# Optimization experiments

Measured on AMD Instinct MI355X. Metric: run time of the kernel, lower is better.

## Reference

```python
import jax, jax.numpy as jnp
import numpy as np

B, S, H, A = 2, 1024, 512, 128


def setup_inputs() -> dict:
    key = jax.random.key(0)
    k1, k2, k3, k4 = jax.random.split(key, 4)
    lstm_output = jax.random.normal(k1, (B, S, H), dtype=jnp.float32)
    w = jax.random.normal(k2, (H, A), dtype=jnp.float32) / np.sqrt(H)
    u = jax.random.normal(k3, (H, A), dtype=jnp.float32) / np.sqrt(H)
    v = jax.random.normal(k4, (A,), dtype=jnp.float32) / np.sqrt(A)
    return {"lstm_output": lstm_output, "w": w, "u": u, "v": v}


def reference(lstm_output, w, u, v):
    # lstm_output: (B,S,H); w,u: (H,A); v: (A,)
    wx = jnp.einsum('bsh,ha->bsa', lstm_output, w)   # (B,S,A)
    ux = jnp.einsum('bsh,ha->bsa', lstm_output, u)   # (B,S,A)
    # e[b,i,j] = tanh(wx[b,i] + ux[b,j]) . v  -> (B,S,S), via (B,S,S,A) intermediate
    e = jnp.einsum('bija,a->bij', jnp.tanh(wx[:, :, None, :] + ux[:, None, :, :]), v)
    attention_weights = jax.nn.softmax(e, axis=-1)   # (B,S,S)
    # bmm(attn, lstm_output) -> (B,S,H), then sum over dim 1 -> (B,H)
    context_vector = jnp.einsum('bij,bjh->bh', attention_weights, lstm_output)
    return context_vector, attention_weights
```

## Files before the change

### kernel.cpp

```cpp
#include <hip/hip_runtime.h>

#define HH   512
#define AA   128
#define SB   1024
#define BATCH 2

__device__ __forceinline__ float fast_rcp(float x) { return __builtin_amdgcn_rcpf(x); }
__device__ __forceinline__ float fast_ex2(float x) { return __builtin_amdgcn_exp2f(x); }

__device__ __forceinline__ void quad_acc(const float4 p, const float4 q4,
                                         const float4 vv, float& acc)
{
    const float d0 = fmaf(p.x, q4.x, 1.0f);
    const float d1 = fmaf(p.y, q4.y, 1.0f);
    const float d2 = fmaf(p.z, q4.z, 1.0f);
    const float d3 = fmaf(p.w, q4.w, 1.0f);
    const float p01 = d0 * d1, p23 = d2 * d3;
    const float na = fmaf(vv.x, d1, vv.y * d0);
    const float nb = fmaf(vv.z, d3, vv.w * d2);
    const float N  = fmaf(na, p23, nb * p01);
    acc = fmaf(N, fast_rcp(p01 * p23), acc);
}

__global__ __launch_bounds__(256) void k1_gemm(const float* __restrict__ lstm,
                                               const float* __restrict__ w,
                                               const float* __restrict__ u,
                                               float* __restrict__ parts,
                                               float* __restrict__ rsum,
                                               float* __restrict__ ctx)
{
    __shared__ float As[16][68];
    __shared__ float Bs[16][68];
    const int t  = threadIdx.x;
    const int bx = blockIdx.x, by = blockIdx.y, bz = blockIdx.z;
    const int m0 = bx * 64;
    const int n0 = by * 64;
    const float* __restrict__ Bsrc = (n0 < AA) ? w : u;
    const int nc = n0 & (AA - 1);

    if (bx == 0) {
        if (by == 0)      { rsum[bz * 512 + t] = 0.f; rsum[bz * 512 + 256 + t] = 0.f; }
        else if (by == 1) { ctx[bz * 256 + t] = 0.f; }
    }

    const int ar = t >> 2, aq = (t & 3) * 4;
    const int bk = t >> 4, bq = (t & 15) * 4;
    const int tm = (t >> 4) * 4, tn = (t & 15) * 4;

    float acc[4][4];
    #pragma unroll
    for (int mi = 0; mi < 4; ++mi)
        #pragma unroll
        for (int ni = 0; ni < 4; ++ni) acc[mi][ni] = 0.f;

    const int kz0 = bz * 128;
    for (int kc = 0; kc < 8; ++kc) {
        const int k0 = kz0 + kc * 16;
        const float4 a4 = *(const float4*)&lstm[(size_t)(m0 + ar) * HH + k0 + aq];
        const float4 b4 = *(const float4*)&Bsrc[(size_t)(k0 + bk) * AA + nc + bq];
        As[aq + 0][ar] = a4.x; As[aq + 1][ar] = a4.y;
        As[aq + 2][ar] = a4.z; As[aq + 3][ar] = a4.w;
        *(float4*)&Bs[bk][bq] = b4;
        __syncthreads();
        #pragma unroll
        for (int k = 0; k < 16; ++k) {
            const float4 av = *(const float4*)&As[k][tm];
            const float4 bv = *(const float4*)&Bs[k][tn];
            #pragma unroll
            for (int mi = 0; mi < 4; ++mi) {
                const float a = (mi == 0) ? av.x : (mi == 1) ? av.y : (mi == 2) ? av.z : av.w;
                acc[mi][0] = fmaf(a, bv.x, acc[mi][0]);
                acc[mi][1] = fmaf(a, bv.y, acc[mi][1]);
                acc[mi][2] = fmaf(a, bv.z, acc[mi][2]);
                acc[mi][3] = fmaf(a, bv.w, acc[mi][3]);
            }
        }
        __syncthreads();
    }

    float* __restrict__ part = parts + (size_t)bz * (2048 * 256);
    #pragma unroll
    for (int mi = 0; mi < 4; ++mi) {
        float4 s; s.x = acc[mi][0]; s.y = acc[mi][1]; s.z = acc[mi][2]; s.w = acc[mi][3];
        *(float4*)&part[(size_t)(m0 + tm + mi) * 256 + n0 + tn] = s;
    }
}

__global__ __launch_bounds__(256) void k1b_combine_exp(const float* __restrict__ parts,
                                                       float* __restrict__ P,
                                                       float* __restrict__ Q)
{
    const float KK = 2.8853900817779268f;
    const int idx = blockIdx.x * 256 + threadIdx.x;
    const float4 c0 = ((const float4*)parts)[idx];
    const float4 c1 = ((const float4*)parts)[idx + 131072];
    const float4 c2 = ((const float4*)parts)[idx + 262144];
    const float4 c3 = ((const float4*)parts)[idx + 393216];
    float4 o;
    o.x = fast_ex2(KK * ((c0.x + c1.x) + (c2.x + c3.x)));
    o.y = fast_ex2(KK * ((c0.y + c1.y) + (c2.y + c3.y)));
    o.z = fast_ex2(KK * ((c0.z + c1.z) + (c2.z + c3.z)));
    o.w = fast_ex2(KK * ((c0.w + c1.w) + (c2.w + c3.w)));
    const int m  = idx >> 6;
    const int qd = idx & 63;
    float* dst = (qd < 32) ? &P[(size_t)m * AA + qd * 4]
                           : &Q[(size_t)m * AA + (qd - 32) * 4];
    *(float4*)dst = o;
}

__global__ __launch_bounds__(256) void k2a_escore(const float* __restrict__ P,
                                                  const float* __restrict__ Q,
                                                  const float* __restrict__ v,
                                                  float* __restrict__ E,
                                                  float* __restrict__ rsum)
{
    const int b  = blockIdx.z;
    const int i0 = blockIdx.y * 8;
    const int j  = blockIdx.x * 256 + threadIdx.x;

    const float4* __restrict__ Qr = (const float4*)&Q[((size_t)b * SB + j) * AA];
    const float*  __restrict__ Pb = &P[((size_t)b * SB + i0) * AA];

    float acc[8];
    #pragma unroll
    for (int i = 0; i < 8; ++i) acc[i] = 0.f;
    float Vacc = 0.f;

    float4 qc[4], qn[4];
    #pragma unroll
    for (int x2 = 0; x2 < 4; ++x2) qc[x2] = Qr[x2];

    for (int xc = 0; xc < 8; ++xc) {
        const int nb4 = (xc < 7) ? (xc + 1) * 4 : 0;
        #pragma unroll
        for (int x2 = 0; x2 < 4; ++x2) qn[x2] = Qr[nb4 + x2];
        #pragma unroll
        for (int x2 = 0; x2 < 4; ++x2) {
            const float4 q4 = qc[x2];
            const float4 vv = *(const float4*)&v[(xc * 4 + x2) * 4];
            Vacc += (vv.x + vv.y) + (vv.z + vv.w);
            #pragma unroll
            for (int i = 0; i < 8; ++i) {
                const float4 p = *(const float4*)&Pb[(size_t)i * AA + (xc * 4 + x2) * 4];
                quad_acc(p, q4, vv, acc[i]);
            }
        }
        #pragma unroll
        for (int x2 = 0; x2 < 4; ++x2) qc[x2] = qn[x2];
    }

    const float L2E  = 1.4426950408889634f;
    const float base = Vacc * L2E;
    float* __restrict__ Eout = &E[((size_t)(b * SB + i0)) * SB + j];
    const int lane = threadIdx.x & 63;
    #pragma unroll
    for (int i = 0; i < 8; ++i) {
        const float e = fast_ex2(fmaf(acc[i], -2.0f * L2E, base));
        Eout[(size_t)i * SB] = e;
        float s = e;
        #pragma unroll
        for (int off = 32; off > 0; off >>= 1) s += __shfl_xor(s, off);
        if (lane == 0) atomicAdd(&rsum[b * SB + i0 + i], s);
    }
}

__global__ __launch_bounds__(1024) void k2b_scale_colpart(float* __restrict__ attn,
                                                          const float* __restrict__ rsum,
                                                          float* __restrict__ colw_part)
{
    const int b  = blockIdx.y;
    const int i0 = blockIdx.x * 8;
    const int j  = threadIdx.x;

    float csum = 0.f;
    #pragma unroll
    for (int i = 0; i < 8; ++i) {
        const int row = b * SB + i0 + i;
        const float inv = fast_rcp(rsum[row]);
        float* __restrict__ ap = &attn[(size_t)row * SB + j];
        const float a = (*ap) * inv;
        *ap = a;
        csum += a;
    }
    colw_part[((size_t)b * 128 + blockIdx.x) * SB + j] = csum;
}

__global__ __launch_bounds__(256) void k4_context(const float* __restrict__ lstm,
                                                  const float* __restrict__ colw_part,
                                                  float* __restrict__ ctx)
{
    const int b  = blockIdx.z;
    const int j0 = blockIdx.y * 32;
    const int h  = blockIdx.x * 256 + threadIdx.x;

    __shared__ float red[8][33];
    __shared__ float cw[32];
    const int jj = threadIdx.x & 31, grp = threadIdx.x >> 5;
    float s = 0.f;
    #pragma unroll
    for (int k2 = 0; k2 < 16; ++k2)
        s += colw_part[((size_t)b * 128 + grp * 16 + k2) * SB + j0 + jj];
    red[grp][jj] = s;
    __syncthreads();
    if (threadIdx.x < 32) {
        float c = 0.f;
        #pragma unroll
        for (int g = 0; g < 8; ++g) c += red[g][threadIdx.x];
        cw[threadIdx.x] = c;
    }
    __syncthreads();

    float acc = 0.f;
    #pragma unroll
    for (int x = 0; x < 32; ++x)
        acc = fmaf(cw[x], lstm[(size_t)(b * SB + j0 + x) * HH + h], acc);
    atomicAdd(&ctx[b * HH + h], acc);
}

extern "C" void kernel_launch(void* const* d_in, const int* in_sizes, int n_in,
                              void* d_out, int out_size, void* d_ws, size_t ws_size,
                              hipStream_t stream)
{
    const float* lstm = (const float*)d_in[0];
    const float* w    = (const float*)d_in[1];
    const float* u    = (const float*)d_in[2];
    const float* v    = (const float*)d_in[3];

    float* out  = (float*)d_out;
    float* ctx  = out;
    float* attn = out + BATCH * HH;

    float* parts     = (float*)d_ws;
    float* P         = parts + (size_t)4 * 2048 * 256;
    float* Qb        = P     + (size_t)BATCH * SB * AA;
    float* rsum      = Qb    + (size_t)BATCH * SB * AA;
    float* colw_part = rsum  + (size_t)BATCH * SB;

    k1_gemm<<<dim3(32, 4, 4), 256, 0, stream>>>(lstm, w, u, parts, rsum, ctx);
    k1b_combine_exp<<<dim3(512), 256, 0, stream>>>(parts, P, Qb);
    k2a_escore<<<dim3(4, 128, BATCH), 256, 0, stream>>>(P, Qb, v, attn, rsum);
    k2b_scale_colpart<<<dim3(128, BATCH), 1024, 0, stream>>>(attn, rsum, colw_part);
    k4_context<<<dim3(2, 32, BATCH), 256, 0, stream>>>(lstm, colw_part, ctx);
}
```

Baseline: 73.72 us.

## Rework GEMM, halve escore rows per block, atomic column sums for context

The projection GEMM drops its shared-memory tiling. Each thread now owns one output column, keeps w/u in prefetched registers and reads lstm rows directly as float4, over a grid of 256x4 blocks. The escore kernel computes 4 rows per block instead of 8, doubling the grid and lowering register pressure, with an occupancy hint added. The column-sum partials become atomicAdds into one colw vector, so k4_context loads colw directly and no longer reduces partials. This trades the partial-buffer traffic and reduction passes for atomic contention and less P reuse per block in escore.

New measurement: 134.8 us. +82.8%, slower.

```diff
diff --git a/kernel.cpp b/kernel.cpp
--- a/kernel.cpp
+++ b/kernel.cpp
@@ -22,68 +22,70 @@
     acc = fmaf(N, fast_rcp(p01 * p23), acc);
 }
 
-__global__ __launch_bounds__(256) void k1_gemm(const float* __restrict__ lstm,
-                                               const float* __restrict__ w,
-                                               const float* __restrict__ u,
-                                               float* __restrict__ parts,
-                                               float* __restrict__ rsum,
-                                               float* __restrict__ ctx)
-{
-    __shared__ float As[16][68];
-    __shared__ float Bs[16][68];
+__global__ __launch_bounds__(256, 8) void k1_gemm(const float* __restrict__ lstm,
+                                                  const float* __restrict__ w,
+                                                  const float* __restrict__ u,
+                                                  float* __restrict__ parts,
+                                                  float* __restrict__ rsum,
+                                                  float* __restrict__ colw,
+                                                  float* __restrict__ ctx)
+{
     const int t  = threadIdx.x;
-    const int bx = blockIdx.x, by = blockIdx.y, bz = blockIdx.z;
-    const int m0 = bx * 64;
-    const int n0 = by * 64;
-    const float* __restrict__ Bsrc = (n0 < AA) ? w : u;
-    const int nc = n0 & (AA - 1);
-
-    if (bx == 0) {
-        if (by == 0)      { rsum[bz * 512 + t] = 0.f; rsum[bz * 512 + 256 + t] = 0.f; }
-        else if (by == 1) { ctx[bz * 256 + t] = 0.f; }
-    }
-
-    const int ar = t >> 2, aq = (t & 3) * 4;
-    const int bk = t >> 4, bq = (t & 15) * 4;
-    const int tm = (t >> 4) * 4, tn = (t & 15) * 4;
-
-    float acc[4][4];
-    #pragma unroll
-    for (int mi = 0; mi < 4; ++mi)
-        #pragma unroll
-        for (int ni = 0; ni < 4; ++ni) acc[mi][ni] = 0.f;
-
-    const int kz0 = bz * 128;
-    for (int kc = 0; kc < 8; ++kc) {
-        const int k0 = kz0 + kc * 16;
-        const float4 a4 = *(const float4*)&lstm[(size_t)(m0 + ar) * HH + k0 + aq];
-        const float4 b4 = *(const float4*)&Bsrc[(size_t)(k0 + bk) * AA + nc + bq];
-        As[aq + 0][ar] = a4.x; As[aq + 1][ar] = a4.y;
-        As[aq + 2][ar] = a4.z; As[aq + 3][ar] = a4.w;
-        *(float4*)&Bs[bk][bq] = b4;
-        __syncthreads();
-        #pragma unroll
-        for (int k = 0; k < 16; ++k) {
-            const float4 av = *(const float4*)&As[k][tm];
-            const float4 bv = *(const float4*)&Bs[k][tn];
-            #pragma unroll
-            for (int mi = 0; mi < 4; ++mi) {
-                const float a = (mi == 0) ? av.x : (mi == 1) ? av.y : (mi == 2) ? av.z : av.w;
-                acc[mi][0] = fmaf(a, bv.x, acc[mi][0]);
-                acc[mi][1] = fmaf(a, bv.y, acc[mi][1]);
-                acc[mi][2] = fmaf(a, bv.z, acc[mi][2]);
-                acc[mi][3] = fmaf(a, bv.w, acc[mi][3]);
-            }
+    const int m0 = blockIdx.x * 8;
+    const int kz = blockIdx.y * 128;
+
+    if (blockIdx.x == 0 && blockIdx.y == 0) {
+        #pragma unroll
+        for (int r = 0; r < 8; ++r) { rsum[r * 256 + t] = 0.f; colw[r * 256 + t] = 0.f; }
+        #pragma unroll
+        for (int r = 0; r < 4; ++r) ctx[r * 256 + t] = 0.f;
+    }
+
+    const float* __restrict__ Bsrc = (t < 128) ? w : u;
+    const int nc = t & (AA - 1);
+
+    float acc[8];
+    #pragma unroll
+    for (int m = 0; m < 8; ++m) acc[m] = 0.f;
+
+    float bc[16], bn[16];
+    #pragma unroll
+    for (int kk = 0; kk < 16; ++kk)
+        bc[kk] = Bsrc[(size_t)(kz + kk) * AA + nc];
+
+    for (int kt = 0; kt < 8; ++kt) {
+        const int knext = (kt < 7) ? (kt + 1) * 16 : 0;
+        #pragma unroll
+        for (int kk = 0; kk < 16; ++kk)
+            bn[kk] = Bsrc[(size_t)(kz + knext + kk) * AA + nc];
+
+        const float* __restrict__ Abase = &lstm[(size_t)m0 * HH + kz + kt * 16];
+        #pragma unroll
+        for (int m = 0; m < 8; ++m) {
+            const float* __restrict__ Am = Abase + (size_t)m * HH;
+            const float4 a0 = *(const float4*)&Am[0];
+            const float4 a1 = *(const float4*)&Am[4];
+            const float4 a2 = *(const float4*)&Am[8];
+            const float4 a3 = *(const float4*)&Am[12];
+            float ac = acc[m];
+            ac = fmaf(a0.x, bc[0],  ac); ac = fmaf(a0.y, bc[1],  ac);
+            ac = fmaf(a0.z, bc[2],  ac); ac = fmaf(a0.w, bc[3],  ac);
+            ac = fmaf(a1.x, bc[4],  ac); ac = fmaf(a1.y, bc[5],  ac);
+            ac = fmaf(a1.z, bc[6],  ac); ac = fmaf(a1.w, bc[7],  ac);
+            ac = fmaf(a2.x, bc[8],  ac); ac = fmaf(a2.y, bc[9],  ac);
+            ac = fmaf(a2.z, bc[10], ac); ac = fmaf(a2.w, bc[11], ac);
+            ac = fmaf(a3.x, bc[12], ac); ac = fmaf(a3.y, bc[13], ac);
+            ac = fmaf(a3.z, bc[14], ac); ac = fmaf(a3.w, bc[15], ac);
+            acc[m] = ac;
         }
-        __syncthreads();
-    }
-
-    float* __restrict__ part = parts + (size_t)bz * (2048 * 256);
-    #pragma unroll
-    for (int mi = 0; mi < 4; ++mi) {
-        float4 s; s.x = acc[mi][0]; s.y = acc[mi][1]; s.z = acc[mi][2]; s.w = acc[mi][3];
-        *(float4*)&part[(size_t)(m0 + tm + mi) * 256 + n0 + tn] = s;
-    }
+        #pragma unroll
+        for (int kk = 0; kk < 16; ++kk) bc[kk] = bn[kk];
+    }
+
+    float* __restrict__ part = parts + (size_t)blockIdx.y * (2048 * 256);
+    #pragma unroll
+    for (int m = 0; m < 8; ++m)
+        part[(size_t)(m0 + m) * 256 + t] = acc[m];
 }
 
 __global__ __launch_bounds__(256) void k1b_combine_exp(const float* __restrict__ parts,
@@ -108,22 +110,22 @@
     *(float4*)dst = o;
 }
 
-__global__ __launch_bounds__(256) void k2a_escore(const float* __restrict__ P,
-                                                  const float* __restrict__ Q,
-                                                  const float* __restrict__ v,
-                                                  float* __restrict__ E,
-                                                  float* __restrict__ rsum)
+__global__ __launch_bounds__(256, 8) void k2a_escore(const float* __restrict__ P,
+                                                     const float* __restrict__ Q,
+                                                     const float* __restrict__ v,
+                                                     float* __restrict__ E,
+                                                     float* __restrict__ rsum)
 {
     const int b  = blockIdx.z;
-    const int i0 = blockIdx.y * 8;
+    const int i0 = blockIdx.y * 4;
     const int j  = blockIdx.x * 256 + threadIdx.x;
 
     const float4* __restrict__ Qr = (const float4*)&Q[((size_t)b * SB + j) * AA];
     const float*  __restrict__ Pb = &P[((size_t)b * SB + i0) * AA];
 
-    float acc[8];
-    #pragma unroll
-    for (int i = 0; i < 8; ++i) acc[i] = 0.f;
+    float acc[4];
+    #pragma unroll
+    for (int i = 0; i < 4; ++i) acc[i] = 0.f;
     float Vacc = 0.f;
 
     float4 qc[4], qn[4];
@@ -140,7 +142,7 @@
             const float4 vv = *(const float4*)&v[(xc * 4 + x2) * 4];
             Vacc += (vv.x + vv.y) + (vv.z + vv.w);
             #pragma unroll
-            for (int i = 0; i < 8; ++i) {
+            for (int i = 0; i < 4; ++i) {
                 const float4 p = *(const float4*)&Pb[(size_t)i * AA + (xc * 4 + x2) * 4];
                 quad_acc(p, q4, vv, acc[i]);
             }
@@ -154,7 +156,7 @@
     float* __restrict__ Eout = &E[((size_t)(b * SB + i0)) * SB + j];
     const int lane = threadIdx.x & 63;
     #pragma unroll
-    for (int i = 0; i < 8; ++i) {
+    for (int i = 0; i < 4; ++i) {
         const float e = fast_ex2(fmaf(acc[i], -2.0f * L2E, base));
         Eout[(size_t)i * SB] = e;
         float s = e;
@@ -164,13 +166,13 @@
     }
 }
 
-__global__ __launch_bounds__(1024) void k2b_scale_colpart(float* __restrict__ attn,
-                                                          const float* __restrict__ rsum,
-                                                          float* __restrict__ colw_part)
-{
-    const int b  = blockIdx.y;
-    const int i0 = blockIdx.x * 8;
-    const int j  = threadIdx.x;
+__global__ __launch_bounds__(256) void k2b_scale_colsum(float* __restrict__ attn,
+                                                        const float* __restrict__ rsum,
+                                                        float* __restrict__ colw)
+{
+    const int b  = blockIdx.z;
+    const int i0 = blockIdx.y * 8;
+    const int j  = blockIdx.x * 256 + threadIdx.x;
 
     float csum = 0.f;
     #pragma unroll
@@ -182,38 +184,23 @@
         *ap = a;
         csum += a;
     }
-    colw_part[((size_t)b * 128 + blockIdx.x) * SB + j] = csum;
+    atomicAdd(&colw[b * SB + j], csum);
 }
 
 __global__ __launch_bounds__(256) void k4_context(const float* __restrict__ lstm,
-                                                  const float* __restrict__ colw_part,
+                                                  const float* __restrict__ colw,
                                                   float* __restrict__ ctx)
 {
     const int b  = blockIdx.z;
-    const int j0 = blockIdx.y * 32;
     const int h  = blockIdx.x * 256 + threadIdx.x;
-
-    __shared__ float red[8][33];
-    __shared__ float cw[32];
-    const int jj = threadIdx.x & 31, grp = threadIdx.x >> 5;
-    float s = 0.f;
-    #pragma unroll
-    for (int k2 = 0; k2 < 16; ++k2)
-        s += colw_part[((size_t)b * 128 + grp * 16 + k2) * SB + j0 + jj];
-    red[grp][jj] = s;
+    const int j0 = blockIdx.y * 128;
+    __shared__ float cw[128];
+    if (threadIdx.x < 128) cw[threadIdx.x] = colw[b * SB + j0 + threadIdx.x];
     __syncthreads();
-    if (threadIdx.x < 32) {
-        float c = 0.f;
-        #pragma unroll
-        for (int g = 0; g < 8; ++g) c += red[g][threadIdx.x];
-        cw[threadIdx.x] = c;
-    }
-    __syncthreads();
-
     float acc = 0.f;
-    #pragma unroll
-    for (int x = 0; x < 32; ++x)
-        acc = fmaf(cw[x], lstm[(size_t)(b * SB + j0 + x) * HH + h], acc);
+    #pragma unroll 8
+    for (int jj = 0; jj < 128; ++jj)
+        acc = fmaf(cw[jj], lstm[(size_t)(b * SB + j0 + jj) * HH + h], acc);
     atomicAdd(&ctx[b * HH + h], acc);
 }
 
@@ -230,15 +217,15 @@
     float* ctx  = out;
     float* attn = out + BATCH * HH;
 
-    float* parts     = (float*)d_ws;
-    float* P         = parts + (size_t)4 * 2048 * 256;
-    float* Qb        = P     + (size_t)BATCH * SB * AA;
-    float* rsum      = Qb    + (size_t)BATCH * SB * AA;
-    float* colw_part = rsum  + (size_t)BATCH * SB;
-
-    k1_gemm<<<dim3(32, 4, 4), 256, 0, stream>>>(lstm, w, u, parts, rsum, ctx);
+    float* parts = (float*)d_ws;
+    float* P     = parts + (size_t)4 * 2048 * 256;
+    float* Qb    = P     + (size_t)BATCH * SB * AA;
+    float* rsum  = Qb    + (size_t)BATCH * SB * AA;
+    float* colw  = rsum  + (size_t)BATCH * SB;
+
+    k1_gemm<<<dim3(256, 4), 256, 0, stream>>>(lstm, w, u, parts, rsum, colw, ctx);
     k1b_combine_exp<<<dim3(512), 256, 0, stream>>>(parts, P, Qb);
-    k2a_escore<<<dim3(4, 128, BATCH), 256, 0, stream>>>(P, Qb, v, attn, rsum);
-    k2b_scale_colpart<<<dim3(128, BATCH), 1024, 0, stream>>>(attn, rsum, colw_part);
-    k4_context<<<dim3(2, 32, BATCH), 256, 0, stream>>>(lstm, colw_part, ctx);
-}
+    k2a_escore<<<dim3(4, 256, BATCH), 256, 0, stream>>>(P, Qb, v, attn, rsum);
+    k2b_scale_colsum<<<dim3(4, 128, BATCH), 256, 0, stream>>>(attn, rsum, colw);
+    k4_context<<<dim3(2, 8, BATCH), 256, 0, stream>>>(lstm, colw, ctx);
+}
```
